# Kernel optimization log

Hardware: AMD Instinct MI355X
Metric: run time of the kernel (lower is better)

Reference implementation:

```python
import jax, jax.numpy as jnp
import numpy as np

N_NODES = 50000
N_EDGES = 800000
D_IN = 128
D_OUT = 128


def setup_inputs() -> dict:
    key = jax.random.key(0)
    k1, k2, k3, k4, k5 = jax.random.split(key, 5)
    x = jax.random.normal(k1, (N_NODES, D_IN), dtype=jnp.float32)
    edge_index = jax.random.randint(k2, (2, N_EDGES), 0, N_NODES, dtype=jnp.int64)
    # PyG SAGEConv params: lin_l (neighbors, with bias), lin_r (root, no bias)
    scale = 1.0 / np.sqrt(D_IN)
    W_l = jax.random.uniform(k3, (D_OUT, D_IN), dtype=jnp.float32, minval=-scale, maxval=scale)
    b_l = jax.random.uniform(k4, (D_OUT,), dtype=jnp.float32, minval=-scale, maxval=scale)
    W_r = jax.random.uniform(k5, (D_OUT, D_IN), dtype=jnp.float32, minval=-scale, maxval=scale)
    return {"x": x, "edge_index": edge_index, "W_l": W_l, "b_l": b_l, "W_r": W_r}


def reference(x, edge_index, W_l, b_l, W_r):
    src, dst = edge_index[0], edge_index[1]
    # mean aggregation of neighbor (source) features into destination nodes
    msg = x[src]  # [E, D_IN]
    agg_sum = jax.ops.segment_sum(msg, dst, num_segments=N_NODES)  # [N, D_IN]
    deg = jax.ops.segment_sum(jnp.ones((N_EDGES,), dtype=x.dtype), dst, num_segments=N_NODES)
    agg = agg_sum / jnp.maximum(deg, 1.0)[:, None]  # isolated nodes -> 0
    # out = lin_l(agg) + lin_r(x); ReLU from SAGE_NET wrapper (active=True)
    out = agg @ W_l.T + b_l + x @ W_r.T
    return jax.nn.relu(out)
```

## Files before the change

### kernel.cpp

```cpp
#include <hip/hip_runtime.h>
#include <hip/hip_bf16.h>

#define NNODES 50000
#define NEDGES 800000
#define DD 128
#define WPITCH 129
#define NPART 8
#define PSIZE 6250
#define CAP 64
#define FILL_B 25000
#define XCV_B 6250
#define WB_B 64

typedef unsigned int u32;
typedef unsigned short u16;
typedef short bf16x8 __attribute__((ext_vector_type(8)));
typedef float f32x4 __attribute__((ext_vector_type(4)));
typedef float f32x2 __attribute__((ext_vector_type(2)));

#if defined(__has_builtin)
#if __has_builtin(__builtin_amdgcn_cvt_pk_f32_fp8)
#define HAVE_HW_FP8 1
#endif
#endif

union U4B8 {
    uint4 u;
    bf16x8 b;
};

__device__ __forceinline__ u32 f2b(float f) {
    u32 u = __float_as_uint(f);
    u32 rounding = 0x7fffu + ((u >> 16) & 1u);
    return (u + rounding) >> 16;
}
__device__ __forceinline__ float blo(u32 v) { return __uint_as_float(v << 16); }
__device__ __forceinline__ float bhi(u32 v) {
    return __uint_as_float(v & 0xffff0000u);
}

__device__ __forceinline__ u32 f2e4m3(float f) {
    u32 u = __float_as_uint(f);
    u32 s = (u >> 31) << 7;
    u32 mag = u & 0x7fffffffu;
    if (mag < 0x3c800000u) return s;
    u32 t = mag + 0x0007FFFFu + ((mag >> 20) & 1u);
    u32 e = (t >> 23) - 120u;
    u32 m = (t >> 20) & 7u;
    if (e > 15u || (e == 15u && m == 7u)) { e = 15u; m = 6u; }
    return s | (e << 3) | m;
}

__device__ __forceinline__ void fp8x4_acc(u32 v, float& a0, float& a1,
                                          float& a2, float& a3) {
#ifdef HAVE_HW_FP8
    f32x2 lo = __builtin_amdgcn_cvt_pk_f32_fp8((int)v, false);
    f32x2 hi = __builtin_amdgcn_cvt_pk_f32_fp8((int)v, true);
    a0 += lo.x;
    a1 += lo.y;
    a2 += hi.x;
    a3 += hi.y;
#else
#pragma unroll
    for (int b = 0; b < 4; ++b) {
        u32 byte = (v >> (8 * b)) & 0xffu;
        u32 f = ((byte >> 7) << 31) | ((((byte >> 3) & 15u) + 120u) << 23) |
                ((byte & 7u) << 20);
        float val = (byte & 0x78u) ? __uint_as_float(f) : 0.f;
        if (b == 0) a0 += val;
        else if (b == 1) a1 += val;
        else if (b == 2) a2 += val;
        else a3 += val;
    }
#endif
}

__global__ __launch_bounds__(256) void work_k(
    const int* __restrict__ ei, u32* __restrict__ deg, u32* __restrict__ slots,
    const float* __restrict__ x, u32* __restrict__ xb, u32* __restrict__ xq,
    const float* __restrict__ Wl, const float* __restrict__ Wr,
    u32* __restrict__ wb) {
    const int b = blockIdx.x, tid = threadIdx.x;
    if (b < FILL_B) {
        u32 part = (u32)b & (NPART - 1);
        u32 e = ((u32)b >> 3) * 256u + tid;
        int dst = ei[NEDGES + e];
        if ((u32)(dst - part * PSIZE) < (u32)PSIZE) {
            u32 pos = atomicAdd(deg + dst, 1u);
            if (pos < CAP) slots[(size_t)dst * CAP + pos] = (u32)ei[e];
        }
    } else if (b < FILL_B + XCV_B) {
        int i = (b - FILL_B) * 256 + tid;
        float4 v = ((const float4*)x)[i];
        uint2 o;
        o.x = f2b(v.x) | (f2b(v.y) << 16);
        o.y = f2b(v.z) | (f2b(v.w) << 16);
        ((uint2*)xb)[i] = o;
        xq[i] = f2e4m3(v.x) | (f2e4m3(v.y) << 8) | (f2e4m3(v.z) << 16) |
                (f2e4m3(v.w) << 24);
    } else {
        int idx = (b - FILL_B - XCV_B) * 256 + tid;
        int o = idx >> 7, c = idx & 127, k0 = 2 * c;
        const float* src = (k0 < DD) ? (Wl + o * DD + k0) : (Wr + o * DD + (k0 - DD));
        wb[idx] = f2b(src[0]) | (f2b(src[1]) << 16);
    }
}

__global__ __launch_bounds__(256) void gather_fp8_k(
    const u32* __restrict__ xq, const u32* __restrict__ slots,
    const u32* __restrict__ deg, u32* __restrict__ aggb) {
    u32 gid = blockIdx.x * 256u + threadIdx.x;
    u32 node = gid >> 6;
    u32 lane = gid & 63u;
    if (node >= NNODES) return;
    u32 d = deg[node];
    u32 cnt = min(d, (u32)CAP);
    u32 sv = slots[(size_t)node * CAP + lane];
    const u32 half = lane >> 5;
    const u32 q = lane & 31u;
    float a0 = 0.f, a1 = 0.f, a2 = 0.f, a3 = 0.f;
    u32 j = 0;
    for (; j + 16 <= cnt; j += 16) {
        u32 v[8];
#pragma unroll
        for (int p = 0; p < 8; ++p) {
            u32 sA = __shfl(sv, (int)(j + 2 * p), 64);
            u32 sB = __shfl(sv, (int)(j + 2 * p + 1), 64);
            u32 s = half ? sB : sA;
            v[p] = xq[(size_t)s * 32 + q];
        }
#pragma unroll
        for (int p = 0; p < 8; ++p) fp8x4_acc(v[p], a0, a1, a2, a3);
    }
    for (; j + 2 <= cnt; j += 2) {
        u32 sA = __shfl(sv, (int)j, 64);
        u32 sB = __shfl(sv, (int)(j + 1), 64);
        u32 s = half ? sB : sA;
        fp8x4_acc(xq[(size_t)s * 32 + q], a0, a1, a2, a3);
    }
    if (j < cnt) {
        u32 sA = __shfl(sv, (int)j, 64);
        u32 v = xq[(size_t)sA * 32 + q];
        if (!half) fp8x4_acc(v, a0, a1, a2, a3);
    }
    a0 += __shfl_xor(a0, 32, 64);
    a1 += __shfl_xor(a1, 32, 64);
    a2 += __shfl_xor(a2, 32, 64);
    a3 += __shfl_xor(a3, 32, 64);
    if (lane < 32) {
        float inv = 1.0f / fmaxf((float)d, 1.0f);
        uint2 o;
        o.x = f2b(a0 * inv) | (f2b(a1 * inv) << 16);
        o.y = f2b(a2 * inv) | (f2b(a3 * inv) << 16);
        *(uint2*)&aggb[(size_t)node * 64 + q * 2] = o;
    }
}

__global__ __launch_bounds__(256) void mfma_fused_k(
    const u32* __restrict__ aggb, const u32* __restrict__ xb,
    const u32* __restrict__ wb, const float* __restrict__ bl,
    float* __restrict__ out) {
    __shared__ u32 w_lds[DD * WPITCH];
    __shared__ float sbias[DD];
    const int tid = threadIdx.x;
    for (int r = tid >> 5; r < DD; r += 8) {
        int c = (tid & 31) * 4;
        uint4 v = *(const uint4*)&wb[r * DD + c];
        *(uint4*)&w_lds[r * WPITCH + c] = v;
    }
    if (tid < DD) sbias[tid] = bl[tid];
    __syncthreads();

    const int wave = tid >> 6, lane = tid & 63;
    const int m = lane & 15, quad = lane >> 4;
    const int row0 = blockIdx.x * 128 + wave * 32;

    f32x4 acc[2][8];
#pragma unroll
    for (int t = 0; t < 2; ++t)
#pragma unroll
        for (int nt = 0; nt < 8; ++nt) acc[t][nt] = (f32x4){0.f, 0.f, 0.f, 0.f};

    for (int ks = 0; ks < 8; ++ks) {
        const u32* A = (ks < 4) ? aggb : xb;
        const int kc = (ks & 3) * 16 + quad * 4;
        U4B8 af[2];
#pragma unroll
        for (int t = 0; t < 2; ++t) {
            int r = row0 + t * 16 + m;
            r = r < NNODES ? r : NNODES - 1;
            af[t].u = *(const uint4*)&A[(size_t)r * 64 + kc];
        }
#pragma unroll
        for (int nt = 0; nt < 8; ++nt) {
            U4B8 bf;
            bf.u = *(const uint4*)&w_lds[(nt * 16 + m) * WPITCH + ks * 16 + quad * 4];
            acc[0][nt] = __builtin_amdgcn_mfma_f32_16x16x32_bf16(
                af[0].b, bf.b, acc[0][nt], 0, 0, 0);
            acc[1][nt] = __builtin_amdgcn_mfma_f32_16x16x32_bf16(
                af[1].b, bf.b, acc[1][nt], 0, 0, 0);
        }
    }
#pragma unroll
    for (int t = 0; t < 2; ++t) {
#pragma unroll
        for (int nt = 0; nt < 8; ++nt) {
            int col = nt * 16 + m;
            float b = sbias[col];
#pragma unroll
            for (int r = 0; r < 4; ++r) {
                int row = row0 + t * 16 + quad * 4 + r;
                if (row < NNODES)
                    out[(size_t)row * DD + col] = fmaxf(acc[t][nt][r] + b, 0.f);
            }
        }
    }
}

__global__ __launch_bounds__(256) void scatter_k(
    const float* __restrict__ x, const int* __restrict__ ei,
    float* __restrict__ agg, u32* __restrict__ deg) {
    u32 gid = blockIdx.x * 256u + threadIdx.x;
    u32 edge = gid >> 6;
    u32 lane = gid & 63u;
    if (edge >= NEDGES) return;
    int src = ei[edge];
    int dst = ei[NEDGES + edge];
    float2 v = ((const float2*)(x + (size_t)src * DD))[lane];
    float* p = agg + (size_t)dst * DD + lane * 2u;
    unsafeAtomicAdd(p, v.x);
    unsafeAtomicAdd(p + 1, v.y);
    if (lane == 0) atomicAdd(deg + dst, 1u);
}

__global__ __launch_bounds__(256) void mean_k(
    float* __restrict__ agg, const u32* __restrict__ deg) {
    u32 gid = blockIdx.x * 256u + threadIdx.x;
    u32 node = gid >> 6;
    u32 lane = gid & 63u;
    if (node >= NNODES) return;
    float inv = 1.0f / fmaxf((float)deg[node], 1.0f);
    float2* p = (float2*)(agg + (size_t)node * DD) + lane;
    float2 v = *p;
    *p = make_float2(v.x * inv, v.y * inv);
}

__global__ __launch_bounds__(256) void lin_l_k(
    float* __restrict__ agg,
    const float* __restrict__ Wl, const float* __restrict__ bl) {
    __shared__ u32 WT[DD * 65];
    __shared__ float rows[4 * DD];
    __shared__ float sbias[DD];
    const int tid = threadIdx.x;
    {
        u16* WTs = (u16*)WT;
        for (int i = tid; i < DD * DD; i += 256) {
            int o = i >> 7, k = i & 127;
            WTs[k * 130 + o] = (u16)f2b(Wl[i]);
        }
        if (tid < DD) sbias[tid] = bl[tid];
    }
    __syncthreads();
    const int h = tid & 63;
    const int nl = tid >> 6;
    for (int base = blockIdx.x * 4; base < NNODES; base += gridDim.x * 4) {
        ((float2*)rows)[tid] =
            ((const float2*)(agg + (size_t)(base + (tid >> 6)) * DD))[tid & 63];
        __syncthreads();
        float acc0 = sbias[2 * h], acc1 = sbias[2 * h + 1];
#pragma unroll
        for (int k = 0; k < DD; ++k) {
            float a = rows[nl * DD + k];
            u32 w2 = WT[k * 65 + h];
            acc0 = fmaf(a, __uint_as_float(w2 << 16), acc0);
            acc1 = fmaf(a, __uint_as_float(w2 & 0xffff0000u), acc1);
        }
        __syncthreads();
        ((float2*)(agg + (size_t)(base + nl) * DD))[h] = make_float2(acc0, acc1);
    }
}

__global__ __launch_bounds__(256) void lin_r_k(
    float* __restrict__ io, const float* __restrict__ x,
    const float* __restrict__ Wr) {
    __shared__ u32 WT[DD * 65];
    __shared__ float rows[4 * DD];
    const int tid = threadIdx.x;
    {
        u16* WTs = (u16*)WT;
        for (int i = tid; i < DD * DD; i += 256) {
            int o = i >> 7, k = i & 127;
            WTs[k * 130 + o] = (u16)f2b(Wr[i]);
        }
    }
    __syncthreads();
    const int h = tid & 63;
    const int nl = tid >> 6;
    for (int base = blockIdx.x * 4; base < NNODES; base += gridDim.x * 4) {
        ((float2*)rows)[tid] =
            ((const float2*)(x + (size_t)(base + (tid >> 6)) * DD))[tid & 63];
        __syncthreads();
        float2 t2 = ((const float2*)(io + (size_t)(base + nl) * DD))[h];
        float acc0 = t2.x, acc1 = t2.y;
#pragma unroll
        for (int k = 0; k < DD; ++k) {
            float a = rows[nl * DD + k];
            u32 w2 = WT[k * 65 + h];
            acc0 = fmaf(a, __uint_as_float(w2 << 16), acc0);
            acc1 = fmaf(a, __uint_as_float(w2 & 0xffff0000u), acc1);
        }
        acc0 = fmaxf(acc0, 0.f);
        acc1 = fmaxf(acc1, 0.f);
        __syncthreads();
        ((float2*)(io + (size_t)(base + nl) * DD))[h] = make_float2(acc0, acc1);
    }
}

extern "C" void kernel_launch(void* const* d_in, const int* in_sizes, int n_in,
                              void* d_out, int out_size, void* d_ws, size_t ws_size,
                              hipStream_t stream) {
    const float* x  = (const float*)d_in[0];
    const int*   ei = (const int*)d_in[1];
    const float* Wl = (const float*)d_in[2];
    const float* bl = (const float*)d_in[3];
    const float* Wr = (const float*)d_in[4];

    u32* deg   = (u32*)d_ws;
    u32* slots = deg + NNODES;
    u32* wb    = slots + (size_t)NNODES * CAP;
    u32* xb    = wb + 16384;
    u32* xq    = xb + (size_t)NNODES * 64;
    u32* aggb  = xq + (size_t)NNODES * 32;
    const size_t need =
        ((size_t)NNODES * (1 + CAP + 64 + 32 + 64) + 16384) * 4;

    if (ws_size >= need) {
        hipMemsetAsync(deg, 0, (size_t)NNODES * sizeof(u32), stream);
        work_k<<<FILL_B + XCV_B + WB_B, 256, 0, stream>>>(
            ei, deg, slots, x, xb, xq, Wl, Wr, wb);
        gather_fp8_k<<<12500, 256, 0, stream>>>(xq, slots, deg, aggb);
        mfma_fused_k<<<(NNODES + 127) / 128, 256, 0, stream>>>(
            aggb, xb, wb, bl, (float*)d_out);
    } else {
        float* agg = (float*)d_out;
        hipMemsetAsync(d_out, 0, (size_t)NNODES * DD * sizeof(float), stream);
        hipMemsetAsync(d_ws, 0, (size_t)NNODES * sizeof(u32), stream);
        scatter_k<<<(NEDGES * 64) / 256, 256, 0, stream>>>(x, ei, agg, deg);
        mean_k<<<(NNODES * 64 + 255) / 256, 256, 0, stream>>>(agg, deg);
        lin_l_k<<<1024, 256, 0, stream>>>(agg, Wl, bl);
        lin_r_k<<<1024, 256, 0, stream>>>(agg, x, Wr);
    }
}
```

Measured before the change: 164.7 us.

## Pack edges into 16-bit pairs and store neighbor slots as u16

A new pre-pass kernel zeroes the degree array, replacing the memset. It also packs each edge's src and dst node ids (both below 65536) into one 32-bit word. The fill phase then reads one packed stream, two edges per thread, and halves its block count. Neighbor slot storage shrinks from u32 to u16, which cuts write and read traffic for the slot table, and the gather only loads valid slots. The cost is an extra kernel launch plus an extra pass that writes and reads the packed edge array.

```diff
diff --git a/kernel.cpp b/kernel.cpp
--- a/kernel.cpp
+++ b/kernel.cpp
@@ -8,7 +8,8 @@
 #define NPART 8
 #define PSIZE 6250
 #define CAP 64
-#define FILL_B 25000
+#define PRE_B 1563
+#define FILL_B 12504
 #define XCV_B 6250
 #define WB_B 64
 
@@ -33,10 +34,6 @@
     u32 u = __float_as_uint(f);
     u32 rounding = 0x7fffu + ((u >> 16) & 1u);
     return (u + rounding) >> 16;
-}
-__device__ __forceinline__ float blo(u32 v) { return __uint_as_float(v << 16); }
-__device__ __forceinline__ float bhi(u32 v) {
-    return __uint_as_float(v & 0xffff0000u);
 }
 
 __device__ __forceinline__ u32 f2e4m3(float f) {
@@ -75,19 +72,43 @@
 #endif
 }
 
+__global__ __launch_bounds__(256) void pre_k(const int* __restrict__ ei,
+                                             u32* __restrict__ ep,
+                                             u32* __restrict__ deg) {
+    u32 gid = blockIdx.x * 256u + threadIdx.x;
+    if (gid < NNODES) deg[gid] = 0u;
+    u32 e0 = gid * 2u;
+    if (e0 < NEDGES) {
+        uint2 s = *(const uint2*)&ei[e0];
+        uint2 d = *(const uint2*)&ei[NEDGES + e0];
+        uint2 o;
+        o.x = (d.x & 0xffffu) | (s.x << 16);
+        o.y = (d.y & 0xffffu) | (s.y << 16);
+        *(uint2*)&ep[e0] = o;
+    }
+}
+
 __global__ __launch_bounds__(256) void work_k(
-    const int* __restrict__ ei, u32* __restrict__ deg, u32* __restrict__ slots,
-    const float* __restrict__ x, u32* __restrict__ xb, u32* __restrict__ xq,
+    const u32* __restrict__ ep, u32* __restrict__ deg,
+    u16* __restrict__ slots16, const float* __restrict__ x,
+    u32* __restrict__ xb, u32* __restrict__ xq,
     const float* __restrict__ Wl, const float* __restrict__ Wr,
     u32* __restrict__ wb) {
     const int b = blockIdx.x, tid = threadIdx.x;
     if (b < FILL_B) {
         u32 part = (u32)b & (NPART - 1);
-        u32 e = ((u32)b >> 3) * 256u + tid;
-        int dst = ei[NEDGES + e];
-        if ((u32)(dst - part * PSIZE) < (u32)PSIZE) {
-            u32 pos = atomicAdd(deg + dst, 1u);
-            if (pos < CAP) slots[(size_t)dst * CAP + pos] = (u32)ei[e];
+        u32 t = ((u32)b >> 3) * 256u + tid;
+        uint2 pp = ((const uint2*)ep)[t];
+        u32 e0 = t * 2u;
+        u32 base = part * PSIZE;
+#pragma unroll
+        for (int k = 0; k < 2; ++k) {
+            u32 v = k ? pp.y : pp.x;
+            u32 dst = v & 0xffffu;
+            if (e0 + (u32)k < NEDGES && (dst - base) < (u32)PSIZE) {
+                u32 pos = atomicAdd(deg + dst, 1u);
+                if (pos < CAP) slots16[(size_t)dst * CAP + pos] = (u16)(v >> 16);
+            }
         }
     } else if (b < FILL_B + XCV_B) {
         int i = (b - FILL_B) * 256 + tid;
@@ -107,7 +128,7 @@
 }
 
 __global__ __launch_bounds__(256) void gather_fp8_k(
-    const u32* __restrict__ xq, const u32* __restrict__ slots,
+    const u32* __restrict__ xq, const u16* __restrict__ slots16,
     const u32* __restrict__ deg, u32* __restrict__ aggb) {
     u32 gid = blockIdx.x * 256u + threadIdx.x;
     u32 node = gid >> 6;
@@ -115,7 +136,7 @@
     if (node >= NNODES) return;
     u32 d = deg[node];
     u32 cnt = min(d, (u32)CAP);
-    u32 sv = slots[(size_t)node * CAP + lane];
+    u32 sv = (lane < cnt) ? (u32)slots16[(size_t)node * CAP + lane] : 0u;
     const u32 half = lane >> 5;
     const u32 q = lane & 31u;
     float a0 = 0.f, a1 = 0.f, a2 = 0.f, a3 = 0.f;
@@ -325,20 +346,22 @@
     const float* bl = (const float*)d_in[3];
     const float* Wr = (const float*)d_in[4];
 
-    u32* deg   = (u32*)d_ws;
-    u32* slots = deg + NNODES;
-    u32* wb    = slots + (size_t)NNODES * CAP;
-    u32* xb    = wb + 16384;
-    u32* xq    = xb + (size_t)NNODES * 64;
-    u32* aggb  = xq + (size_t)NNODES * 32;
+    u32* deg     = (u32*)d_ws;
+    u16* slots16 = (u16*)(deg + NNODES);
+    u32* ep      = (u32*)d_ws + NNODES + (size_t)NNODES * CAP / 2;
+    u32* wb      = ep + NEDGES + 256;
+    u32* xb      = wb + 16384;
+    u32* xq      = xb + (size_t)NNODES * 64;
+    u32* aggb    = xq + (size_t)NNODES * 32;
     const size_t need =
-        ((size_t)NNODES * (1 + CAP + 64 + 32 + 64) + 16384) * 4;
+        ((size_t)NNODES * (1 + CAP / 2 + 64 + 32 + 64) + NEDGES + 256 + 16384) *
+        4;
 
     if (ws_size >= need) {
-        hipMemsetAsync(deg, 0, (size_t)NNODES * sizeof(u32), stream);
+        pre_k<<<PRE_B, 256, 0, stream>>>(ei, ep, deg);
         work_k<<<FILL_B + XCV_B + WB_B, 256, 0, stream>>>(
-            ei, deg, slots, x, xb, xq, Wl, Wr, wb);
-        gather_fp8_k<<<12500, 256, 0, stream>>>(xq, slots, deg, aggb);
+            ep, deg, slots16, x, xb, xq, Wl, Wr, wb);
+        gather_fp8_k<<<12500, 256, 0, stream>>>(xq, slots16, deg, aggb);
         mfma_fused_k<<<(NNODES + 127) / 128, 256, 0, stream>>>(
             aggb, xb, wb, bl, (float*)d_out);
     } else {
```

Result: slower. 169.2 us (+2.7%).

## Pack neighbor slots as 16-bit indices and drop partitioned edge fill

Applied to the files above, without the earlier changes.

The adjacency slot table now stores source indices as 16-bit values, filled with atomicOr into a zeroed buffer, which halves the slot memory and its traffic in the gather. The eight-way dst-partitioned fill that reread edge_index eight times is replaced by one pass in which each thread handles two edges with vector loads. The memset grows to also clear the slot table. Node ids up to 50000 fit in 16 bits, and gather now masks unused lanes to zero.

```diff
diff --git a/kernel.cpp b/kernel.cpp
--- a/kernel.cpp
+++ b/kernel.cpp
@@ -5,11 +5,9 @@
 #define NEDGES 800000
 #define DD 128
 #define WPITCH 129
-#define NPART 8
-#define PSIZE 6250
 #define CAP 64
-#define FILL_B 25000
 #define XCV_B 6250
+#define FILL_B 1563
 #define WB_B 64
 
 typedef unsigned int u32;
@@ -33,10 +31,6 @@
     u32 u = __float_as_uint(f);
     u32 rounding = 0x7fffu + ((u >> 16) & 1u);
     return (u + rounding) >> 16;
-}
-__device__ __forceinline__ float blo(u32 v) { return __uint_as_float(v << 16); }
-__device__ __forceinline__ float bhi(u32 v) {
-    return __uint_as_float(v & 0xffff0000u);
 }
 
 __device__ __forceinline__ u32 f2e4m3(float f) {
@@ -81,16 +75,8 @@
     const float* __restrict__ Wl, const float* __restrict__ Wr,
     u32* __restrict__ wb) {
     const int b = blockIdx.x, tid = threadIdx.x;
-    if (b < FILL_B) {
-        u32 part = (u32)b & (NPART - 1);
-        u32 e = ((u32)b >> 3) * 256u + tid;
-        int dst = ei[NEDGES + e];
-        if ((u32)(dst - part * PSIZE) < (u32)PSIZE) {
-            u32 pos = atomicAdd(deg + dst, 1u);
-            if (pos < CAP) slots[(size_t)dst * CAP + pos] = (u32)ei[e];
-        }
-    } else if (b < FILL_B + XCV_B) {
-        int i = (b - FILL_B) * 256 + tid;
+    if (b < XCV_B) {
+        int i = b * 256 + tid;
         float4 v = ((const float4*)x)[i];
         uint2 o;
         o.x = f2b(v.x) | (f2b(v.y) << 16);
@@ -98,8 +84,22 @@
         ((uint2*)xb)[i] = o;
         xq[i] = f2e4m3(v.x) | (f2e4m3(v.y) << 8) | (f2e4m3(v.z) << 16) |
                 (f2e4m3(v.w) << 24);
+    } else if (b < XCV_B + FILL_B) {
+        u32 t = (u32)(b - XCV_B) * 256u + tid;
+        if (t < (u32)(NEDGES / 2)) {
+            uint2 s = ((const uint2*)ei)[t];
+            uint2 d = ((const uint2*)(ei + NEDGES))[t];
+            u32 pos = atomicAdd(deg + d.x, 1u);
+            if (pos < CAP)
+                atomicOr(slots + (size_t)d.x * 32 + (pos >> 1),
+                         s.x << ((pos & 1) * 16));
+            pos = atomicAdd(deg + d.y, 1u);
+            if (pos < CAP)
+                atomicOr(slots + (size_t)d.y * 32 + (pos >> 1),
+                         s.y << ((pos & 1) * 16));
+        }
     } else {
-        int idx = (b - FILL_B - XCV_B) * 256 + tid;
+        int idx = (b - XCV_B - FILL_B) * 256 + tid;
         int o = idx >> 7, c = idx & 127, k0 = 2 * c;
         const float* src = (k0 < DD) ? (Wl + o * DD + k0) : (Wr + o * DD + (k0 - DD));
         wb[idx] = f2b(src[0]) | (f2b(src[1]) << 16);
@@ -107,7 +107,7 @@
 }
 
 __global__ __launch_bounds__(256) void gather_fp8_k(
-    const u32* __restrict__ xq, const u32* __restrict__ slots,
+    const u32* __restrict__ xq, const u16* __restrict__ slots16,
     const u32* __restrict__ deg, u32* __restrict__ aggb) {
     u32 gid = blockIdx.x * 256u + threadIdx.x;
     u32 node = gid >> 6;
@@ -115,7 +115,7 @@
     if (node >= NNODES) return;
     u32 d = deg[node];
     u32 cnt = min(d, (u32)CAP);
-    u32 sv = slots[(size_t)node * CAP + lane];
+    u32 sv = (lane < cnt) ? (u32)slots16[(size_t)node * CAP + lane] : 0u;
     const u32 half = lane >> 5;
     const u32 q = lane & 31u;
     float a0 = 0.f, a1 = 0.f, a2 = 0.f, a3 = 0.f;
@@ -327,18 +327,19 @@
 
     u32* deg   = (u32*)d_ws;
     u32* slots = deg + NNODES;
-    u32* wb    = slots + (size_t)NNODES * CAP;
+    u32* wb    = slots + (size_t)NNODES * (CAP / 2);
     u32* xb    = wb + 16384;
     u32* xq    = xb + (size_t)NNODES * 64;
     u32* aggb  = xq + (size_t)NNODES * 32;
     const size_t need =
-        ((size_t)NNODES * (1 + CAP + 64 + 32 + 64) + 16384) * 4;
+        ((size_t)NNODES * (1 + CAP / 2 + 64 + 32 + 64) + 16384) * 4;
 
     if (ws_size >= need) {
-        hipMemsetAsync(deg, 0, (size_t)NNODES * sizeof(u32), stream);
-        work_k<<<FILL_B + XCV_B + WB_B, 256, 0, stream>>>(
+        hipMemsetAsync(d_ws, 0,
+                       (size_t)NNODES * (1 + CAP / 2) * sizeof(u32), stream);
+        work_k<<<XCV_B + FILL_B + WB_B, 256, 0, stream>>>(
             ei, deg, slots, x, xb, xq, Wl, Wr, wb);
-        gather_fp8_k<<<12500, 256, 0, stream>>>(xq, slots, deg, aggb);
+        gather_fp8_k<<<12500, 256, 0, stream>>>(xq, (const u16*)slots, deg, aggb);
         mfma_fused_k<<<(NNODES + 127) / 128, 256, 0, stream>>>(
             aggb, xb, wb, bl, (float*)d_out);
     } else {
```

After: 200.5 us. 1.22x slower.
